# Kernel tuning notes

Hardware: AMD Instinct MI355X
Metric: run time of the kernel (lower is better)

Reference implementation:

```python
import jax, jax.numpy as jnp
import numpy as np

B, T, D, H, E, R = 4, 1024, 1024, 16, 3, 8
DK = D // H
LORA_SCALE = 1.0 / R  # lora_alpha / lora_rank with alpha=1.0


def mole(x, W, b, A, Bm, Rt):
    """Mixture-of-LoRA-experts linear. x:[b,t,D] -> ([b,t,D], router weights [b,t,E])."""
    w = jax.nn.softmax(x @ Rt, axis=-1)                      # [b,t,E] per-token routing
    base = x @ W.T + b                                        # dense base projection
    u = jnp.einsum('btd,edr->betr', x, A)                     # low-rank down-proj per expert
    lora = jnp.einsum('betr,erf,bte->btf', u, Bm, w)          # up-proj + router-weighted combine
    return base + LORA_SCALE * lora, w


def _mole_params(key, name, out):
    k = jax.random.split(key, 4)
    out[name + '_W'] = 0.02 * jax.random.normal(k[0], (D, D), jnp.float32)
    out[name + '_b'] = jnp.zeros((D,), jnp.float32)
    out[name + '_A'] = 0.02 * jax.random.normal(k[1], (E, D, R), jnp.float32)
    out[name + '_B'] = 0.02 * jax.random.normal(k[2], (E, R, D), jnp.float32)
    out[name + '_R'] = 0.02 * jax.random.normal(k[3], (D, E), jnp.float32)


def setup_inputs() -> dict:
    key = jax.random.key(0)
    ks = jax.random.split(key, 8)
    inp = {
        'query': jax.random.normal(ks[0], (B, T, D), jnp.float32),
        'key': jax.random.normal(ks[1], (B, T, D), jnp.float32),
        'value': jax.random.normal(ks[2], (B, T, D), jnp.float32),
        'mask': jnp.ones((B, 1, T), jnp.bool_),
    }
    for i, name in enumerate(['q', 'k', 'v', 'o']):
        _mole_params(ks[3 + i], name, inp)
    return inp


def reference(query, key, value, mask,
              q_W, q_b, q_A, q_B, q_R,
              k_W, k_b, k_A, k_B, k_R,
              v_W, v_b, v_A, v_B, v_R,
              o_W, o_b, o_A, o_B, o_R):
    nb = query.shape[0]
    q, _ = mole(query, q_W, q_b, q_A, q_B, q_R)
    k, _ = mole(key, k_W, k_b, k_A, k_B, k_R)
    v, _ = mole(value, v_W, v_b, v_A, v_B, v_R)
    # (b, t, D) -> (b, H, t, DK)
    q = q.reshape(nb, -1, H, DK).transpose(0, 2, 1, 3)
    k = k.reshape(nb, -1, H, DK).transpose(0, 2, 1, 3)
    v = v.reshape(nb, -1, H, DK).transpose(0, 2, 1, 3)
    scores = jnp.einsum('bhqd,bhkd->bhqk', q, k) / np.sqrt(DK).astype(np.float32)
    m = (mask[:, None, :, :] == 0)                            # [b,1,1,t2] or [b,1,t1,t2]
    min_val = jnp.finfo(scores.dtype).min
    scores = jnp.where(m, min_val, scores)
    attn = jax.nn.softmax(scores, axis=-1)
    attn = jnp.where(m, 0.0, attn)
    x = jnp.einsum('bhqk,bhkd->bhqd', attn, v)
    x = x.transpose(0, 2, 1, 3).reshape(nb, -1, H * DK)
    out, _ = mole(x, o_W, o_b, o_A, o_B, o_R)
    return out
```

## Files before the change

kernel.cpp:

```cpp
#include <hip/hip_runtime.h>
#include <math.h>

#define BATCH 4
#define SEQ   1024
#define DDIM  1024
#define NH    16
#define HD    64
#define NEXP  3
#define LRANK 8
#define NCOEF 24
#define TOK   4096
#define LSCALE 0.125f
#define DSQ   (DDIM*DDIM)

typedef __attribute__((ext_vector_type(8))) short short8;
typedef __attribute__((ext_vector_type(8))) _Float16 half8;
typedef __attribute__((ext_vector_type(4))) float f32x4;

#if defined(__has_builtin)
#if __has_builtin(__builtin_amdgcn_global_load_lds)
#define HAS_GLDS 1
#endif
#endif

__device__ __forceinline__ void stage16(const void* g, void* lds_base, int lane) {
#ifdef HAS_GLDS
  __builtin_amdgcn_global_load_lds(
      (const __attribute__((address_space(1))) unsigned int*)g,
      (__attribute__((address_space(3))) unsigned int*)lds_base, 16, 0, 0);
#else
  float4 v = *(const float4*)g;
  *(float4*)((char*)lds_base + (size_t)lane * 16) = v;
#endif
}

__device__ __forceinline__ short bf16_rne(float f) {
  unsigned b = __float_as_uint(f);
  return (short)((b + 0x7fffu + ((b >> 16) & 1u)) >> 16);
}
__device__ __forceinline__ short fp16_bits(float f) {
  _Float16 h = (_Float16)f;
  return __builtin_bit_cast(short, h);
}
__device__ __forceinline__ void fp16_split(float f, short& h, short& l) {
  _Float16 hh = (_Float16)f;
  h = __builtin_bit_cast(short, hh);
  _Float16 ll = (_Float16)(f - (float)hh);
  l = __builtin_bit_cast(short, ll);
}

__global__ __launch_bounds__(256) void prep_kernel(
    const float* __restrict__ q_W, const float* __restrict__ k_W,
    const float* __restrict__ v_W, const float* __restrict__ o_W,
    const float* __restrict__ xq, const float* __restrict__ xk,
    const float* __restrict__ xv,
    const float* __restrict__ A0, const float* __restrict__ A1,
    const float* __restrict__ A2, const float* __restrict__ A3,
    const float* __restrict__ R0, const float* __restrict__ R1,
    const float* __restrict__ R2, const float* __restrict__ R3,
    short* __restrict__ WF,
    short* __restrict__ WoH, short* __restrict__ WoL,
    short* __restrict__ Xf3,
    short* __restrict__ Ac)
{
  int bid = blockIdx.x;
  if (bid < 4096) {
    int which = bid >> 10;
    const float* w = (which == 0) ? q_W : (which == 1) ? k_W : (which == 2) ? v_W : o_W;
    size_t i = (size_t)(bid & 1023) * 256 + threadIdx.x;
    float4 v = ((const float4*)w)[i];
    float f[4] = {v.x, v.y, v.z, v.w};
    if (which < 3) {
      short4 hh;
      hh.x = fp16_bits(f[0]); hh.y = fp16_bits(f[1]);
      hh.z = fp16_bits(f[2]); hh.w = fp16_bits(f[3]);
      ((short4*)(WF + (size_t)which * DSQ))[i] = hh;
    } else {
      short hs[4], ls[4];
#pragma unroll
      for (int j = 0; j < 4; ++j) fp16_split(f[j], hs[j], ls[j]);
      short4 hh, ll;
      hh.x = hs[0]; hh.y = hs[1]; hh.z = hs[2]; hh.w = hs[3];
      ll.x = ls[0]; ll.y = ls[1]; ll.z = ls[2]; ll.w = ls[3];
      ((short4*)WoH)[i] = hh;
      ((short4*)WoL)[i] = ll;
    }
  } else if (bid < 16384) {
    int r = bid - 4096;
    int p = r >> 12;
    const float* x = (p == 0) ? xq : (p == 1) ? xk : xv;
    size_t i = (size_t)(r & 4095) * 256 + threadIdx.x;
    float4 v = ((const float4*)x)[i];
    short4 hh;
    hh.x = fp16_bits(v.x); hh.y = fp16_bits(v.y);
    hh.z = fp16_bits(v.z); hh.w = fp16_bits(v.w);
    ((short4*)(Xf3 + (size_t)p * TOK * DDIM))[i] = hh;
  } else {
    int r = bid - 16384;
    int p = r >> 6, bx = r & 63;
    const float* A  = (p == 0) ? A0 : (p == 1) ? A1 : (p == 2) ? A2 : A3;
    const float* Rt = (p == 0) ? R0 : (p == 1) ? R1 : (p == 2) ? R2 : R3;
    short* dst = Ac + (size_t)p * 32 * DDIM;
    int j = threadIdx.x & 31;
#pragma unroll
    for (int dl = 0; dl < 2; ++dl) {
      int d = bx * 16 + dl * 8 + (threadIdx.x >> 5);
      float v = 0.f;
      if (j < 24)      v = A[(size_t)(j >> 3) * DDIM * LRANK + (size_t)d * LRANK + (j & 7)];
      else if (j < 27) v = Rt[(size_t)d * 3 + (j - 24)];
      dst[(size_t)j * DDIM + d] = fp16_bits(v);
    }
  }
}

__global__ __launch_bounds__(256) void coeff_mfma(
    const short* __restrict__ XfB,
    const short* __restrict__ AcB,
    float* __restrict__ CB)
{
  __shared__ float Us[4][16][33];

  const int p = blockIdx.y;
  const short* Xf = XfB + (size_t)p * TOK * DDIM;
  const short* Ac = AcB + (size_t)p * 32 * DDIM;
  float* C = CB + (size_t)p * TOK * NCOEF;
  const int t0 = blockIdx.x * 16;

  const int tid = threadIdx.x, lane = tid & 63, wv = tid >> 6;
  const int lrow = lane & 15, lq = lane >> 4;

  f32x4 acc[2] = {};
  const int k0 = wv * 256 + lq * 8;
#pragma unroll
  for (int kc = 0; kc < 8; ++kc) {
    int k = k0 + kc * 32;
    half8 a8 = *(const half8*)(Xf + (size_t)(t0 + lrow) * DDIM + k);
#pragma unroll
    for (int ng = 0; ng < 2; ++ng) {
      half8 b8 = *(const half8*)(Ac + (size_t)(ng * 16 + lrow) * DDIM + k);
      acc[ng] = __builtin_amdgcn_mfma_f32_16x16x32_f16(a8, b8, acc[ng], 0, 0, 0);
    }
  }

#pragma unroll
  for (int ng = 0; ng < 2; ++ng)
#pragma unroll
    for (int r = 0; r < 4; ++r)
      Us[wv][lq * 4 + r][ng * 16 + lrow] = acc[ng][r];
  __syncthreads();

  int tt = tid >> 4, cc = tid & 15;
  float u0 = Us[0][tt][cc]      + Us[1][tt][cc]      + Us[2][tt][cc]      + Us[3][tt][cc];
  float u1 = Us[0][tt][cc + 16] + Us[1][tt][cc + 16] + Us[2][tt][cc + 16] + Us[3][tt][cc + 16];
  __syncthreads();
  Us[0][tt][cc] = u0;
  Us[0][tt][cc + 16] = u1;
  __syncthreads();

  if (cc < 3) {
    float l0 = Us[0][tt][24], l1 = Us[0][tt][25], l2 = Us[0][tt][26];
    float mx = fmaxf(l0, fmaxf(l1, l2));
    float e0 = __expf(l0 - mx), e1 = __expf(l1 - mx), e2 = __expf(l2 - mx);
    float we = ((cc == 0) ? e0 : (cc == 1) ? e1 : e2) * (LSCALE / (e0 + e1 + e2));
    float* crow = C + (size_t)(t0 + tt) * NCOEF + cc * 8;
#pragma unroll
    for (int i = 0; i < 8; ++i) crow[i] = we * Us[0][tt][cc * 8 + i];
  }
}

__global__ __launch_bounds__(512, 4) void qkv_gemm(
    const short* __restrict__ Xf3,
    const short* __restrict__ WF,
    const float* __restrict__ qb, const float* __restrict__ kb, const float* __restrict__ vb,
    const float* __restrict__ qB, const float* __restrict__ kB, const float* __restrict__ vB,
    const float* __restrict__ C3,
    short* __restrict__ qf, short* __restrict__ kf,
    short* __restrict__ vtf)
{
  __shared__ __align__(16) short SMEM[2][16384];

  const int id = blockIdx.x;
  const int xcd = id & 7, j = id >> 3;
  const int proj = j >> 5, r2 = j & 31;
  const int t0 = (xcd * 4 + (r2 >> 3)) * 128;
  const int f0 = (r2 & 7) * 128;

  const short* Xf = Xf3 + (size_t)proj * ((size_t)TOK * DDIM);
  const short* Wf = WF + (size_t)proj * DSQ;
  const float* bias = (proj == 0) ? qb : (proj == 1) ? kb : vb;
  const float* Bm   = (proj == 0) ? qB : (proj == 1) ? kB : vB;
  const float* C = C3 + (size_t)proj * TOK * NCOEF;

  const int tid = threadIdx.x, lane = tid & 63, wave = tid >> 6;
  const int wm = wave >> 1, wn = wave & 1;
  const int lrow = lane & 15, lq = lane >> 4;

  const short* gsrc[4]; int loff[4];
#pragma unroll
  for (int i = 0; i < 4; ++i) {
    int sid = wave * 4 + i;
    int kind = sid >> 4, c = sid & 15;
    int row = (c >> 1) * 16 + lrow, koff = (c & 1) * 32 + lq * 8;
    if (kind == 0) { gsrc[i] = Xf + (size_t)(t0 + row) * DDIM + koff; loff[i] = c * 512; }
    else           { gsrc[i] = Wf + (size_t)(f0 + row) * DDIM + koff; loff[i] = 8192 + c * 512; }
  }

  f32x4 acc[2][4] = {};

#pragma unroll
  for (int i = 0; i < 4; ++i) stage16(gsrc[i], &SMEM[0][loff[i]], lane);
  __syncthreads();

  for (int it = 0; it < 16; ++it) {
    const int cur = it & 1;
    if (it < 15) {
      int kk = (it + 1) * 64;
#pragma unroll
      for (int i = 0; i < 4; ++i) stage16(gsrc[i] + kk, &SMEM[cur ^ 1][loff[i]], lane);
    }
    const short* As = SMEM[cur];
    const short* Bs = SMEM[cur] + 8192;
#pragma unroll
    for (int kf2 = 0; kf2 < 2; ++kf2) {
      half8 a8[2], b8[4];
#pragma unroll
      for (int mt = 0; mt < 2; ++mt)
        a8[mt] = *(const half8*)(As + ((wm*2 + mt)*2 + kf2) * 512 + lane * 8);
#pragma unroll
      for (int nt = 0; nt < 4; ++nt)
        b8[nt] = *(const half8*)(Bs + ((wn*4 + nt)*2 + kf2) * 512 + lane * 8);
#pragma unroll
      for (int mt = 0; mt < 2; ++mt)
#pragma unroll
        for (int nt = 0; nt < 4; ++nt)
          acc[mt][nt] = __builtin_amdgcn_mfma_f32_16x16x32_f16(a8[mt], b8[nt], acc[mt][nt], 0, 0, 0);
    }
    __syncthreads();
  }

  short* LC = SMEM[0];
  short* LB = SMEM[0] + 128 * 40;
  for (int idx = tid; idx < 128 * 32; idx += 512) {
    int r = idx >> 5, jj = idx & 31;
    LC[r * 40 + jj] = (jj < NCOEF) ? bf16_rne(C[(size_t)(t0 + r) * NCOEF + jj]) : (short)0;
    LB[r * 40 + jj] = (jj < NCOEF) ? bf16_rne(Bm[(size_t)jj * DDIM + f0 + r]) : (short)0;
  }
  __syncthreads();

  short8 cf[2], bfr[4];
#pragma unroll
  for (int mt = 0; mt < 2; ++mt)
    cf[mt] = *(const short8*)(LC + (wm*32 + mt*16 + lrow) * 40 + lq * 8);
#pragma unroll
  for (int nt = 0; nt < 4; ++nt)
    bfr[nt] = *(const short8*)(LB + (wn*64 + nt*16 + lrow) * 40 + lq * 8);
#pragma unroll
  for (int mt = 0; mt < 2; ++mt)
#pragma unroll
    for (int nt = 0; nt < 4; ++nt)
      acc[mt][nt] = __builtin_amdgcn_mfma_f32_16x16x32_bf16(cf[mt], bfr[nt], acc[mt][nt], 0, 0, 0);

  if (proj < 2) {
    short* Y = (proj == 0) ? qf : kf;
#pragma unroll
    for (int nt = 0; nt < 4; ++nt) {
      const int f = f0 + wn*64 + nt*16 + lrow;
      const float bv = bias[f];
#pragma unroll
      for (int mt = 0; mt < 2; ++mt)
#pragma unroll
        for (int r = 0; r < 4; ++r) {
          int t = t0 + wm*32 + mt*16 + lq*4 + r;
          Y[(size_t)t * DDIM + f] = fp16_bits(acc[mt][nt][r] + bv);
        }
    }
  } else {
    short4 hv[2][4];
#pragma unroll
    for (int nt = 0; nt < 4; ++nt) {
      const float bv = bias[f0 + wn*64 + nt*16 + lrow];
#pragma unroll
      for (int mt = 0; mt < 2; ++mt) {
        short4 h4;
        h4.x = fp16_bits(acc[mt][nt][0] + bv);
        h4.y = fp16_bits(acc[mt][nt][1] + bv);
        h4.z = fp16_bits(acc[mt][nt][2] + bv);
        h4.w = fp16_bits(acc[mt][nt][3] + bv);
        hv[mt][nt] = h4;
      }
    }
    short* T = SMEM[0];
    __syncthreads();
#pragma unroll
    for (int pass = 0; pass < 2; ++pass) {
      if (wn == pass) {
#pragma unroll
        for (int nt = 0; nt < 4; ++nt)
#pragma unroll
          for (int mt = 0; mt < 2; ++mt)
            *(short4*)(T + (nt*16 + lrow) * 132 + wm*32 + mt*16 + lq*4) = hv[mt][nt];
      }
      __syncthreads();
      int r = tid >> 3, ch = (tid & 7) * 16;
      short* dst = vtf + (size_t)(f0 + pass*64 + r) * TOK + t0 + ch;
      const short* src = T + r * 132 + ch;
      *(float4*)(dst) = *(const float4*)(src);
      *(float4*)(dst + 8) = *(const float4*)(src + 8);
      __syncthreads();
    }
  }
}

__global__ __launch_bounds__(512, 4) void o_gemm(
    const short* __restrict__ Xh,
    const short* __restrict__ Wh, const short* __restrict__ Wl,
    const float* __restrict__ bias,
    const float* __restrict__ Bm,
    const float* __restrict__ C,
    float* __restrict__ Y)
{
  __shared__ __align__(16) short SMEM[2][10240];

  const int id = blockIdx.x;
  const int xcd = id & 7, j = id >> 3;
  const int t0 = (xcd * 8 + (j >> 3)) * 64;
  const int f0 = (j & 7) * 128;

  const int tid = threadIdx.x, lane = tid & 63, wave = tid >> 6;
  const int wm = wave >> 2, wn = wave & 3;
  const int lrow = lane & 15, lq = lane >> 4;

  const short* gsrc[3]; int loff[3]; int nst = 0;
  {
    const short* bases[3] = {Xh, Wh, Wl};
#pragma unroll
    for (int i = 0; i < 3; ++i) {
      int sid = wave * 3 + i;
      if (sid < 20) {
        int kind, c;
        if (sid < 4)       { kind = 0; c = sid; }
        else if (sid < 12) { kind = 1; c = sid - 4; }
        else               { kind = 2; c = sid - 12; }
        int r0 = (kind == 0) ? t0 : f0;
        gsrc[nst] = bases[kind] + (size_t)(r0 + c * 16 + lrow) * DDIM + lq * 8;
        loff[nst] = ((kind == 0) ? 0 : (kind == 1) ? 2048 : 6144) + c * 512;
        ++nst;
      }
    }
  }

  f32x4 acc[2][2] = {};

  for (int i = 0; i < nst; ++i) stage16(gsrc[i], &SMEM[0][loff[i]], lane);
  __syncthreads();

  for (int it = 0; it < 32; ++it) {
    const int cur = it & 1;
    if (it < 31) {
      int kk = (it + 1) * 32;
      for (int i = 0; i < nst; ++i) stage16(gsrc[i] + kk, &SMEM[cur ^ 1][loff[i]], lane);
    }
    const short* As = SMEM[cur];
    const short* Bh = SMEM[cur] + 2048;
    const short* Bl = SMEM[cur] + 6144;
    half8 a8[2], b8h[2], b8l[2];
#pragma unroll
    for (int mt = 0; mt < 2; ++mt)
      a8[mt] = *(const half8*)(As + (wm*2 + mt) * 512 + lane * 8);
#pragma unroll
    for (int nt = 0; nt < 2; ++nt) {
      b8h[nt] = *(const half8*)(Bh + (wn*2 + nt) * 512 + lane * 8);
      b8l[nt] = *(const half8*)(Bl + (wn*2 + nt) * 512 + lane * 8);
    }
#pragma unroll
    for (int mt = 0; mt < 2; ++mt)
#pragma unroll
      for (int nt = 0; nt < 2; ++nt) {
        acc[mt][nt] = __builtin_amdgcn_mfma_f32_16x16x32_f16(a8[mt], b8h[nt], acc[mt][nt], 0, 0, 0);
        acc[mt][nt] = __builtin_amdgcn_mfma_f32_16x16x32_f16(a8[mt], b8l[nt], acc[mt][nt], 0, 0, 0);
      }
    __syncthreads();
  }

  short* LC = SMEM[0];
  short* LB = SMEM[0] + 64 * 40;
  for (int idx = tid; idx < 64 * 32; idx += 512) {
    int r = idx >> 5, jj = idx & 31;
    LC[r * 40 + jj] = (jj < NCOEF) ? bf16_rne(C[(size_t)(t0 + r) * NCOEF + jj]) : (short)0;
  }
  for (int idx = tid; idx < 128 * 32; idx += 512) {
    int r = idx >> 5, jj = idx & 31;
    LB[r * 40 + jj] = (jj < NCOEF) ? bf16_rne(Bm[(size_t)jj * DDIM + f0 + r]) : (short)0;
  }
  __syncthreads();

  short8 cf[2], bfr[2];
#pragma unroll
  for (int mt = 0; mt < 2; ++mt)
    cf[mt] = *(const short8*)(LC + (wm*32 + mt*16 + lrow) * 40 + lq * 8);
#pragma unroll
  for (int nt = 0; nt < 2; ++nt)
    bfr[nt] = *(const short8*)(LB + (wn*32 + nt*16 + lrow) * 40 + lq * 8);
#pragma unroll
  for (int mt = 0; mt < 2; ++mt)
#pragma unroll
    for (int nt = 0; nt < 2; ++nt)
      acc[mt][nt] = __builtin_amdgcn_mfma_f32_16x16x32_bf16(cf[mt], bfr[nt], acc[mt][nt], 0, 0, 0);

#pragma unroll
  for (int nt = 0; nt < 2; ++nt) {
    const int f = f0 + wn*32 + nt*16 + lrow;
    const float bv = bias[f];
#pragma unroll
    for (int mt = 0; mt < 2; ++mt)
#pragma unroll
      for (int r = 0; r < 4; ++r) {
        int t = t0 + wm*32 + mt*16 + lq*4 + r;
        Y[(size_t)t * DDIM + f] = acc[mt][nt][r] + bv;
      }
  }
}

__global__ __launch_bounds__(512, 4) void attn_mfma(
    const short* __restrict__ Qf,
    const short* __restrict__ Kf,
    const short* __restrict__ VTf,
    short* __restrict__ Xh)
{
  __shared__ __align__(16) short KV[2][8192];
  __shared__ __align__(16) short Ps[8][2][16 * 40];

  const int tid  = threadIdx.x;
  const int lane = tid & 63, wv = tid >> 6;
  const int lrow = lane & 15, lq = lane >> 4;

  const int id = blockIdx.x;
  const int xcd = id & 7, j = id >> 3;
  const int bh = xcd * 8 + (j >> 3);
  const int qt = j & 7;
  const int b = bh >> 4, hh = bh & 15;

  half8 qfr[2];
  {
    size_t qrow = (size_t)(b * SEQ + qt * 128 + wv * 16 + lrow);
#pragma unroll
    for (int c = 0; c < 2; ++c)
      qfr[c] = *(const half8*)(Qf + qrow * DDIM + hh*64 + c*32 + lq*8);
  }

  const short* gsrc[2]; int loff[2]; int gstep[2];
#pragma unroll
  for (int i = 0; i < 2; ++i) {
    int sid = wv * 2 + i;
    int kind = sid >> 3, c = sid & 7;
    int rg = c >> 1, dk = c & 1;
    if (kind == 0) {
      gsrc[i] = Kf + (size_t)(b * SEQ + rg * 16 + lrow) * DDIM + hh*64 + dk*32 + lq*8;
      gstep[i] = 64 * DDIM;
      loff[i] = c * 512;
    } else {
      gsrc[i] = VTf + (size_t)(hh*64 + rg*16 + lrow) * TOK + b * SEQ + dk*32 + lq*8;
      gstep[i] = 64;
      loff[i] = 4096 + c * 512;
    }
  }

  f32x4 oacc[4] = {};
  float ps[4] = {};

#pragma unroll
  for (int i = 0; i < 2; ++i) stage16(gsrc[i], &KV[0][loff[i]], lane);
  __syncthreads();

  for (int kt = 0; kt < SEQ / 64; ++kt) {
    const int cur = kt & 1;
    if (kt < SEQ / 64 - 1) {
#pragma unroll
      for (int i = 0; i < 2; ++i)
        stage16(gsrc[i] + (size_t)(kt + 1) * gstep[i], &KV[cur ^ 1][loff[i]], lane);
    }
    const short* Ks = KV[cur];
    const short* Vs = KV[cur] + 4096;

    f32x4 s[4] = {};
#pragma unroll
    for (int nt = 0; nt < 4; ++nt)
#pragma unroll
      for (int c = 0; c < 2; ++c) {
        half8 b8 = *(const half8*)(Ks + (nt*2 + c) * 512 + lane * 8);
        s[nt] = __builtin_amdgcn_mfma_f32_16x16x32_f16(qfr[c], b8, s[nt], 0, 0, 0);
      }

#pragma unroll
    for (int nt = 0; nt < 4; ++nt)
#pragma unroll
      for (int r = 0; r < 4; ++r) {
        float p = __expf(s[nt][r] * 0.125f);
        ps[r] += p;
        Ps[wv][nt >> 1][(4*lq + r)*40 + (nt & 1)*16 + lrow] = fp16_bits(p);
      }

#pragma unroll
    for (int c = 0; c < 2; ++c) {
      half8 pa = *(const half8*)(&Ps[wv][c][lrow*40 + lq*8]);
#pragma unroll
      for (int nt = 0; nt < 4; ++nt) {
        half8 v8 = *(const half8*)(Vs + (nt*2 + c) * 512 + lane * 8);
        oacc[nt] = __builtin_amdgcn_mfma_f32_16x16x32_f16(pa, v8, oacc[nt], 0, 0, 0);
      }
    }
    __syncthreads();
  }

#pragma unroll
  for (int r = 0; r < 4; ++r) {
#pragma unroll
    for (int m = 1; m < 16; m <<= 1) ps[r] += __shfl_xor(ps[r], m, 64);
  }

#pragma unroll
  for (int r = 0; r < 4; ++r) {
    float inv = 1.f / ps[r];
    size_t t = (size_t)(b * SEQ + qt * 128 + wv * 16 + 4*lq + r);
#pragma unroll
    for (int nt = 0; nt < 4; ++nt) {
      int d = hh*64 + nt*16 + lrow;
      Xh[t * DDIM + d] = fp16_bits(oacc[nt][r] * inv);
    }
  }
}

extern "C" void kernel_launch(void* const* d_in, const int* in_sizes, int n_in,
                              void* d_out, int out_size, void* d_ws, size_t ws_size,
                              hipStream_t stream) {
  const float* query = (const float*)d_in[0];
  const float* key   = (const float*)d_in[1];
  const float* value = (const float*)d_in[2];
  const float* q_W = (const float*)d_in[4];
  const float* q_b = (const float*)d_in[5];
  const float* q_A = (const float*)d_in[6];
  const float* q_B = (const float*)d_in[7];
  const float* q_R = (const float*)d_in[8];
  const float* k_W = (const float*)d_in[9];
  const float* k_b = (const float*)d_in[10];
  const float* k_A = (const float*)d_in[11];
  const float* k_B = (const float*)d_in[12];
  const float* k_R = (const float*)d_in[13];
  const float* v_W = (const float*)d_in[14];
  const float* v_b = (const float*)d_in[15];
  const float* v_A = (const float*)d_in[16];
  const float* v_B = (const float*)d_in[17];
  const float* v_R = (const float*)d_in[18];
  const float* o_W = (const float*)d_in[19];
  const float* o_b = (const float*)d_in[20];
  const float* o_A = (const float*)d_in[21];
  const float* o_B = (const float*)d_in[22];
  const float* o_R = (const float*)d_in[23];

  float* out = (float*)d_out;

  const size_t NBUF = (size_t)TOK * DDIM;
  char* w = (char*)d_ws;
  float* cbuf = (float*)w;                 w += (size_t)4 * TOK * NCOEF * 4;
  short* Xf3  = (short*)w;                 w += 3 * NBUF * 2;
  short* qfb  = (short*)w;                 w += NBUF * 2;
  short* kfb  = (short*)w;                 w += NBUF * 2;
  short* vtf  = (short*)w;                 w += NBUF * 2;
  short* WF   = (short*)w;                 w += (size_t)3 * DSQ * 2;
  short* WoH  = (short*)w;                 w += (size_t)DSQ * 2;
  short* WoL  = (short*)w;                 w += (size_t)DSQ * 2;
  short* AcF  = (short*)w;
  short* iXh = Xf3;

  dim3 gCf3(TOK / 16, 3);
  dim3 gCf1(TOK / 16, 1);

  prep_kernel<<<16640, 256, 0, stream>>>(q_W, k_W, v_W, o_W, query, key, value,
                                         q_A, k_A, v_A, o_A, q_R, k_R, v_R, o_R,
                                         WF, WoH, WoL, Xf3, AcF);
  coeff_mfma<<<gCf3, 256, 0, stream>>>(Xf3, AcF, cbuf);
  qkv_gemm<<<768, 512, 0, stream>>>(Xf3, WF, q_b, k_b, v_b,
                                    q_B, k_B, v_B, cbuf, qfb, kfb, vtf);
  attn_mfma<<<512, 512, 0, stream>>>(qfb, kfb, vtf, iXh);
  coeff_mfma<<<gCf1, 256, 0, stream>>>(iXh, AcF + (size_t)3 * 32 * DDIM,
                                       cbuf + (size_t)3 * TOK * NCOEF);
  o_gemm<<<512, 512, 0, stream>>>(iXh, WoH, WoL,
                                  o_b, o_B, cbuf + (size_t)3 * TOK * NCOEF, out);
}
```

Before: 310.4 us.

## Split K across wave groups in QKV and O GEMMs with LDS reduction

Both the QKV projection GEMM and the output GEMM now split each 64-wide K step between two groups of four waves. Each wave computes a larger 2D output sub-tile over half the K slice, which raises register reuse of loaded fragments. The two partial accumulators are then reduced through LDS, and each group finishes half of the N tiles. The O GEMM also doubles its K step to 64 with larger LDS buffers, halving the number of loop iterations and barriers. The cost is more accumulator registers, more LDS per block (which may reduce occupancy), and an extra LDS exchange with barriers.

```diff
diff --git a/kernel.cpp b/kernel.cpp
--- a/kernel.cpp
+++ b/kernel.cpp
@@ -192,7 +192,8 @@
   const float* C = C3 + (size_t)proj * TOK * NCOEF;
 
   const int tid = threadIdx.x, lane = tid & 63, wave = tid >> 6;
-  const int wm = wave >> 1, wn = wave & 1;
+  const int kg = wave >> 2;
+  const int w2 = wave & 3, wm = w2 >> 1, wn = w2 & 1;
   const int lrow = lane & 15, lq = lane >> 4;
 
   const short* gsrc[4]; int loff[4];
@@ -205,7 +206,7 @@
     else           { gsrc[i] = Wf + (size_t)(f0 + row) * DDIM + koff; loff[i] = 8192 + c * 512; }
   }
 
-  f32x4 acc[2][4] = {};
+  f32x4 acc[4][4] = {};
 
 #pragma unroll
   for (int i = 0; i < 4; ++i) stage16(gsrc[i], &SMEM[0][loff[i]], lane);
@@ -220,23 +221,50 @@
     }
     const short* As = SMEM[cur];
     const short* Bs = SMEM[cur] + 8192;
-#pragma unroll
-    for (int kf2 = 0; kf2 < 2; ++kf2) {
-      half8 a8[2], b8[4];
-#pragma unroll
-      for (int mt = 0; mt < 2; ++mt)
-        a8[mt] = *(const half8*)(As + ((wm*2 + mt)*2 + kf2) * 512 + lane * 8);
+    half8 a8[4], b8[4];
+#pragma unroll
+    for (int mt = 0; mt < 4; ++mt)
+      a8[mt] = *(const half8*)(As + ((wm*4 + mt)*2 + kg) * 512 + lane * 8);
+#pragma unroll
+    for (int nt = 0; nt < 4; ++nt)
+      b8[nt] = *(const half8*)(Bs + ((wn*4 + nt)*2 + kg) * 512 + lane * 8);
+#pragma unroll
+    for (int mt = 0; mt < 4; ++mt)
 #pragma unroll
       for (int nt = 0; nt < 4; ++nt)
-        b8[nt] = *(const half8*)(Bs + ((wn*4 + nt)*2 + kf2) * 512 + lane * 8);
-#pragma unroll
-      for (int mt = 0; mt < 2; ++mt)
-#pragma unroll
-        for (int nt = 0; nt < 4; ++nt)
-          acc[mt][nt] = __builtin_amdgcn_mfma_f32_16x16x32_f16(a8[mt], b8[nt], acc[mt][nt], 0, 0, 0);
-    }
+        acc[mt][nt] = __builtin_amdgcn_mfma_f32_16x16x32_f16(a8[mt], b8[nt], acc[mt][nt], 0, 0, 0);
     __syncthreads();
   }
+
+  {
+    float4* xch = (float4*)&SMEM[0][0];
+    float4* dst = xch + ((w2 * 2 + kg) * 512) + lane;
+#pragma unroll
+    for (int mt = 0; mt < 4; ++mt)
+#pragma unroll
+      for (int jj = 0; jj < 2; ++jj) {
+        int nt = 2 * (kg ^ 1) + jj;
+        float4 v;
+        v.x = acc[mt][nt][0]; v.y = acc[mt][nt][1];
+        v.z = acc[mt][nt][2]; v.w = acc[mt][nt][3];
+        dst[(mt * 2 + jj) * 64] = v;
+      }
+  }
+  __syncthreads();
+  {
+    const float4* xch = (const float4*)&SMEM[0][0];
+    const float4* src = xch + ((w2 * 2 + (kg ^ 1)) * 512) + lane;
+#pragma unroll
+    for (int mt = 0; mt < 4; ++mt)
+#pragma unroll
+      for (int jj = 0; jj < 2; ++jj) {
+        int nt = 2 * kg + jj;
+        float4 v = src[(mt * 2 + jj) * 64];
+        acc[mt][nt][0] += v.x; acc[mt][nt][1] += v.y;
+        acc[mt][nt][2] += v.z; acc[mt][nt][3] += v.w;
+      }
+  }
+  __syncthreads();
 
   short* LC = SMEM[0];
   short* LB = SMEM[0] + 128 * 40;
@@ -247,46 +275,48 @@
   }
   __syncthreads();
 
-  short8 cf[2], bfr[4];
-#pragma unroll
-  for (int mt = 0; mt < 2; ++mt)
-    cf[mt] = *(const short8*)(LC + (wm*32 + mt*16 + lrow) * 40 + lq * 8);
-#pragma unroll
-  for (int nt = 0; nt < 4; ++nt)
-    bfr[nt] = *(const short8*)(LB + (wn*64 + nt*16 + lrow) * 40 + lq * 8);
-#pragma unroll
-  for (int mt = 0; mt < 2; ++mt)
-#pragma unroll
-    for (int nt = 0; nt < 4; ++nt)
-      acc[mt][nt] = __builtin_amdgcn_mfma_f32_16x16x32_bf16(cf[mt], bfr[nt], acc[mt][nt], 0, 0, 0);
+  short8 cf[4], bfr[2];
+#pragma unroll
+  for (int mt = 0; mt < 4; ++mt)
+    cf[mt] = *(const short8*)(LC + (wm*64 + mt*16 + lrow) * 40 + lq * 8);
+#pragma unroll
+  for (int jj = 0; jj < 2; ++jj)
+    bfr[jj] = *(const short8*)(LB + (wn*64 + (2*kg + jj)*16 + lrow) * 40 + lq * 8);
+#pragma unroll
+  for (int mt = 0; mt < 4; ++mt)
+#pragma unroll
+    for (int jj = 0; jj < 2; ++jj)
+      acc[mt][2*kg + jj] = __builtin_amdgcn_mfma_f32_16x16x32_bf16(cf[mt], bfr[jj], acc[mt][2*kg + jj], 0, 0, 0);
 
   if (proj < 2) {
     short* Y = (proj == 0) ? qf : kf;
 #pragma unroll
-    for (int nt = 0; nt < 4; ++nt) {
+    for (int jj = 0; jj < 2; ++jj) {
+      const int nt = 2*kg + jj;
       const int f = f0 + wn*64 + nt*16 + lrow;
       const float bv = bias[f];
 #pragma unroll
-      for (int mt = 0; mt < 2; ++mt)
+      for (int mt = 0; mt < 4; ++mt)
 #pragma unroll
         for (int r = 0; r < 4; ++r) {
-          int t = t0 + wm*32 + mt*16 + lq*4 + r;
+          int t = t0 + wm*64 + mt*16 + lq*4 + r;
           Y[(size_t)t * DDIM + f] = fp16_bits(acc[mt][nt][r] + bv);
         }
     }
   } else {
-    short4 hv[2][4];
-#pragma unroll
-    for (int nt = 0; nt < 4; ++nt) {
+    short4 hv[4][2];
+#pragma unroll
+    for (int jj = 0; jj < 2; ++jj) {
+      const int nt = 2*kg + jj;
       const float bv = bias[f0 + wn*64 + nt*16 + lrow];
 #pragma unroll
-      for (int mt = 0; mt < 2; ++mt) {
+      for (int mt = 0; mt < 4; ++mt) {
         short4 h4;
         h4.x = fp16_bits(acc[mt][nt][0] + bv);
         h4.y = fp16_bits(acc[mt][nt][1] + bv);
         h4.z = fp16_bits(acc[mt][nt][2] + bv);
         h4.w = fp16_bits(acc[mt][nt][3] + bv);
-        hv[mt][nt] = h4;
+        hv[mt][jj] = h4;
       }
     }
     short* T = SMEM[0];
@@ -295,10 +325,10 @@
     for (int pass = 0; pass < 2; ++pass) {
       if (wn == pass) {
 #pragma unroll
-        for (int nt = 0; nt < 4; ++nt)
-#pragma unroll
-          for (int mt = 0; mt < 2; ++mt)
-            *(short4*)(T + (nt*16 + lrow) * 132 + wm*32 + mt*16 + lq*4) = hv[mt][nt];
+        for (int jj = 0; jj < 2; ++jj)
+#pragma unroll
+          for (int mt = 0; mt < 4; ++mt)
+            *(short4*)(T + ((2*kg + jj)*16 + lrow) * 132 + wm*64 + mt*16 + lq*4) = hv[mt][jj];
       }
       __syncthreads();
       int r = tid >> 3, ch = (tid & 7) * 16;
@@ -319,7 +349,7 @@
     const float* __restrict__ C,
     float* __restrict__ Y)
 {
-  __shared__ __align__(16) short SMEM[2][10240];
+  __shared__ __align__(16) short SMEM[2][20480];
 
   const int id = blockIdx.x;
   const int xcd = id & 7, j = id >> 3;
@@ -327,60 +357,86 @@
   const int f0 = (j & 7) * 128;
 
   const int tid = threadIdx.x, lane = tid & 63, wave = tid >> 6;
-  const int wm = wave >> 2, wn = wave & 3;
+  const int kg = wave >> 2;
+  const int w2 = wave & 3, wm = w2 >> 1, wn = w2 & 1;
   const int lrow = lane & 15, lq = lane >> 4;
 
-  const short* gsrc[3]; int loff[3]; int nst = 0;
-  {
-    const short* bases[3] = {Xh, Wh, Wl};
-#pragma unroll
-    for (int i = 0; i < 3; ++i) {
-      int sid = wave * 3 + i;
-      if (sid < 20) {
-        int kind, c;
-        if (sid < 4)       { kind = 0; c = sid; }
-        else if (sid < 12) { kind = 1; c = sid - 4; }
-        else               { kind = 2; c = sid - 12; }
-        int r0 = (kind == 0) ? t0 : f0;
-        gsrc[nst] = bases[kind] + (size_t)(r0 + c * 16 + lrow) * DDIM + lq * 8;
-        loff[nst] = ((kind == 0) ? 0 : (kind == 1) ? 2048 : 6144) + c * 512;
-        ++nst;
-      }
-    }
-  }
-
-  f32x4 acc[2][2] = {};
-
-  for (int i = 0; i < nst; ++i) stage16(gsrc[i], &SMEM[0][loff[i]], lane);
-  __syncthreads();
-
-  for (int it = 0; it < 32; ++it) {
+  const short* gsrc[5]; int loff[5];
+#pragma unroll
+  for (int i = 0; i < 5; ++i) {
+    int sid = wave * 5 + i;
+    const short* base; int r0, c, off0;
+    if (sid < 8)       { base = Xh; r0 = t0; c = sid;      off0 = 0; }
+    else if (sid < 24) { base = Wh; r0 = f0; c = sid - 8;  off0 = 4096; }
+    else               { base = Wl; r0 = f0; c = sid - 24; off0 = 12288; }
+    gsrc[i] = base + (size_t)(r0 + (c >> 1) * 16 + lrow) * DDIM + (c & 1) * 32 + lq * 8;
+    loff[i] = off0 + c * 512;
+  }
+
+  f32x4 acc[2][4] = {};
+
+#pragma unroll
+  for (int i = 0; i < 5; ++i) stage16(gsrc[i], &SMEM[0][loff[i]], lane);
+  __syncthreads();
+
+  for (int it = 0; it < 16; ++it) {
     const int cur = it & 1;
-    if (it < 31) {
-      int kk = (it + 1) * 32;
-      for (int i = 0; i < nst; ++i) stage16(gsrc[i] + kk, &SMEM[cur ^ 1][loff[i]], lane);
+    if (it < 15) {
+      int kk = (it + 1) * 64;
+#pragma unroll
+      for (int i = 0; i < 5; ++i) stage16(gsrc[i] + kk, &SMEM[cur ^ 1][loff[i]], lane);
     }
     const short* As = SMEM[cur];
-    const short* Bh = SMEM[cur] + 2048;
-    const short* Bl = SMEM[cur] + 6144;
-    half8 a8[2], b8h[2], b8l[2];
+    const short* Bh = SMEM[cur] + 4096;
+    const short* Bl = SMEM[cur] + 12288;
+    half8 a8[2], b8h[4], b8l[4];
 #pragma unroll
     for (int mt = 0; mt < 2; ++mt)
-      a8[mt] = *(const half8*)(As + (wm*2 + mt) * 512 + lane * 8);
-#pragma unroll
-    for (int nt = 0; nt < 2; ++nt) {
-      b8h[nt] = *(const half8*)(Bh + (wn*2 + nt) * 512 + lane * 8);
-      b8l[nt] = *(const half8*)(Bl + (wn*2 + nt) * 512 + lane * 8);
+      a8[mt] = *(const half8*)(As + ((wm*2 + mt)*2 + kg) * 512 + lane * 8);
+#pragma unroll
+    for (int nt = 0; nt < 4; ++nt) {
+      b8h[nt] = *(const half8*)(Bh + ((wn*4 + nt)*2 + kg) * 512 + lane * 8);
+      b8l[nt] = *(const half8*)(Bl + ((wn*4 + nt)*2 + kg) * 512 + lane * 8);
     }
 #pragma unroll
     for (int mt = 0; mt < 2; ++mt)
 #pragma unroll
-      for (int nt = 0; nt < 2; ++nt) {
+      for (int nt = 0; nt < 4; ++nt) {
         acc[mt][nt] = __builtin_amdgcn_mfma_f32_16x16x32_f16(a8[mt], b8h[nt], acc[mt][nt], 0, 0, 0);
         acc[mt][nt] = __builtin_amdgcn_mfma_f32_16x16x32_f16(a8[mt], b8l[nt], acc[mt][nt], 0, 0, 0);
       }
     __syncthreads();
   }
+
+  {
+    float4* xch = (float4*)&SMEM[0][0];
+    float4* dst = xch + ((w2 * 2 + kg) * 256) + lane;
+#pragma unroll
+    for (int mt = 0; mt < 2; ++mt)
+#pragma unroll
+      for (int jj = 0; jj < 2; ++jj) {
+        int nt = 2 * (kg ^ 1) + jj;
+        float4 v;
+        v.x = acc[mt][nt][0]; v.y = acc[mt][nt][1];
+        v.z = acc[mt][nt][2]; v.w = acc[mt][nt][3];
+        dst[(mt * 2 + jj) * 64] = v;
+      }
+  }
+  __syncthreads();
+  {
+    const float4* xch = (const float4*)&SMEM[0][0];
+    const float4* src = xch + ((w2 * 2 + (kg ^ 1)) * 256) + lane;
+#pragma unroll
+    for (int mt = 0; mt < 2; ++mt)
+#pragma unroll
+      for (int jj = 0; jj < 2; ++jj) {
+        int nt = 2 * kg + jj;
+        float4 v = src[(mt * 2 + jj) * 64];
+        acc[mt][nt][0] += v.x; acc[mt][nt][1] += v.y;
+        acc[mt][nt][2] += v.z; acc[mt][nt][3] += v.w;
+      }
+  }
+  __syncthreads();
 
   short* LC = SMEM[0];
   short* LB = SMEM[0] + 64 * 40;
@@ -399,17 +455,18 @@
   for (int mt = 0; mt < 2; ++mt)
     cf[mt] = *(const short8*)(LC + (wm*32 + mt*16 + lrow) * 40 + lq * 8);
 #pragma unroll
-  for (int nt = 0; nt < 2; ++nt)
-    bfr[nt] = *(const short8*)(LB + (wn*32 + nt*16 + lrow) * 40 + lq * 8);
+  for (int jj = 0; jj < 2; ++jj)
+    bfr[jj] = *(const short8*)(LB + (wn*64 + (2*kg + jj)*16 + lrow) * 40 + lq * 8);
 #pragma unroll
   for (int mt = 0; mt < 2; ++mt)
 #pragma unroll
-    for (int nt = 0; nt < 2; ++nt)
-      acc[mt][nt] = __builtin_amdgcn_mfma_f32_16x16x32_bf16(cf[mt], bfr[nt], acc[mt][nt], 0, 0, 0);
-
-#pragma unroll
-  for (int nt = 0; nt < 2; ++nt) {
-    const int f = f0 + wn*32 + nt*16 + lrow;
+    for (int jj = 0; jj < 2; ++jj)
+      acc[mt][2*kg + jj] = __builtin_amdgcn_mfma_f32_16x16x32_bf16(cf[mt], bfr[jj], acc[mt][2*kg + jj], 0, 0, 0);
+
+#pragma unroll
+  for (int jj = 0; jj < 2; ++jj) {
+    const int nt = 2*kg + jj;
+    const int f = f0 + wn*64 + nt*16 + lrow;
     const float bv = bias[f];
 #pragma unroll
     for (int mt = 0; mt < 2; ++mt)
```

Measured after the change: 847.2 us. +172.9%, slower.
